# Performance work log

Hardware: AMD Instinct MI355X
Metric: run time of the kernel (lower is better)

Reference implementation:

```python
import jax, jax.numpy as jnp
import numpy as np

N_HEADS = 16


def _rope_table(seq_len, head_dim):
    # Matches RotaryPositionalEmbedding: emb = cat(sin(pos*inv_freq), cos(pos*inv_freq))
    inv_freq = 1.0 / (10000.0 ** (jnp.arange(0, head_dim, 2, dtype=jnp.float32) / head_dim))
    sinusoid = jnp.arange(seq_len, dtype=jnp.float32)[:, None] * inv_freq[None, :]  # [S, hd/2]
    return jnp.sin(sinusoid), jnp.cos(sinusoid)


def _apply_rope(q, k, seq_len, head_dim):
    # Faithful to the torch code, which slices emb[:, :hd/2] (== sin) and calls it 'cos',
    # and emb[:, hd/2:] (== cos) and calls it 'sin'. We keep that exact math.
    sin_tab, cos_tab = _rope_table(seq_len, head_dim)
    c = sin_tab[None, None]  # named 'cos' in torch code, actually sin values
    s = cos_tab[None, None]  # named 'sin' in torch code, actually cos values
    half = head_dim // 2
    def rot(x):
        x1, x2 = x[..., :half], x[..., half:]
        return jnp.concatenate([x1 * c - x2 * s, x2 * c + x1 * s], axis=-1)
    return rot(q), rot(k)


def setup_inputs() -> dict:
    key = jax.random.key(0)
    ks = jax.random.split(key, 9)
    B, S, D = 4, 2048, 1024
    sc = 1.0 / np.sqrt(D)
    return {
        'hidden_states': jax.random.normal(ks[0], (B, S, D), jnp.float32),
        'Wq': jax.random.normal(ks[1], (D, D), jnp.float32) * sc,
        'bq': jax.random.normal(ks[2], (D,), jnp.float32) * 0.01,
        'Wk': jax.random.normal(ks[3], (D, D), jnp.float32) * sc,
        'bk': jax.random.normal(ks[4], (D,), jnp.float32) * 0.01,
        'Wv': jax.random.normal(ks[5], (D, D), jnp.float32) * sc,
        'bv': jax.random.normal(ks[6], (D,), jnp.float32) * 0.01,
        'Wo': jax.random.normal(ks[7], (D, D), jnp.float32) * sc,
        'bo': jax.random.normal(ks[8], (D,), jnp.float32) * 0.01,
    }


def reference(hidden_states, Wq, bq, Wk, bk, Wv, bv, Wo, bo):
    B, S, D = hidden_states.shape
    H = N_HEADS
    hd = D // H

    def proj(W, b):
        y = jnp.einsum('bsd,ed->bse', hidden_states, W) + b  # nn.Linear: x @ W.T + b
        return y.reshape(B, S, H, hd).transpose(0, 2, 1, 3)   # [B,H,S,hd]

    q = proj(Wq, bq)
    k = proj(Wk, bk)
    v = proj(Wv, bv)
    q, k = _apply_rope(q, k, S, hd)

    scale = 1.0 / np.sqrt(hd)
    scores = jnp.einsum('bhqd,bhkd->bhqk', q, k) * scale  # [B,H,S,S]
    attn = jax.nn.softmax(scores, axis=-1)
    ctx = jnp.einsum('bhqk,bhkd->bhqd', attn, v)          # [B,H,S,hd]
    ctx = ctx.transpose(0, 2, 1, 3).reshape(B, S, D)
    return jnp.einsum('bsd,ed->bse', ctx, Wo) + bo
```

## Files before the change

### kernel.cpp

```cpp
#include <hip/hip_runtime.h>
#include <math.h>

#define SEQ 2048
#define DMODEL 1024
#define NH 16
#define HD 64
#define BH 64
#define MROWS 8192
#define QKV_U16 8388608
#define LOG2E 1.4426950408889634f

typedef __attribute__((ext_vector_type(8))) _Float16 half8;
typedef __attribute__((ext_vector_type(4))) _Float16 half4;
typedef __attribute__((ext_vector_type(2))) __fp16 fp16v2;
typedef __attribute__((ext_vector_type(8))) short short8;
typedef __attribute__((ext_vector_type(4))) float floatx4;
typedef unsigned short ush;

union FH { _Float16 h; ush u; };
union PK { fp16v2 v; unsigned u; };
union PH { unsigned u[2]; half4 h; };

__device__ inline ush f2h(float x) { FH c; c.h = (_Float16)x; return c.u; }

__device__ inline void glds16(const ush* g, ush* l) {
  __builtin_amdgcn_global_load_lds((const __attribute__((address_space(1))) void*)g,
                                   (__attribute__((address_space(3))) void*)l, 16, 0, 0);
}

__global__ __launch_bounds__(256)
void cvt_kb(const float* __restrict__ src, ush* __restrict__ dst, int M) {
  __shared__ float T[64][33];
  const int t = threadIdx.x;
  const int k0 = blockIdx.x * 32, m0 = blockIdx.y * 64;
  {
    int row = t >> 2, c = (t & 3) * 8;
    const float* sp = src + (size_t)(m0 + row) * DMODEL + k0 + c;
    float4 x0 = *(const float4*)sp;
    float4 x1 = *(const float4*)(sp + 4);
    float xs[8] = {x0.x, x0.y, x0.z, x0.w, x1.x, x1.y, x1.z, x1.w};
#pragma unroll
    for (int j = 0; j < 8; ++j) T[row][c + j] = xs[j];
  }
  __syncthreads();
  const int ml = t & 63, kbl = t >> 6;
  short8 h8;
#pragma unroll
  for (int j = 0; j < 8; ++j) h8[j] = (short)f2h(T[ml][kbl * 8 + j]);
  *(short8*)(dst + ((size_t)(k0 / 8 + kbl) * M + m0 + ml) * 8) = h8;
}

__global__ __launch_bounds__(256)
void cvt_w4(const float* __restrict__ W0, const float* __restrict__ W1,
            const float* __restrict__ W2, const float* __restrict__ W3,
            ush* __restrict__ dst) {
  __shared__ float T[64][33];
  const int z = blockIdx.z;
  const float* src = (z == 0) ? W0 : (z == 1) ? W1 : (z == 2) ? W2 : W3;
  ush* dz = dst + (size_t)z * DMODEL * DMODEL;
  const int t = threadIdx.x;
  const int k0 = blockIdx.x * 32, m0 = blockIdx.y * 64;
  {
    int row = t >> 2, c = (t & 3) * 8;
    const float* sp = src + (size_t)(m0 + row) * DMODEL + k0 + c;
    float4 x0 = *(const float4*)sp;
    float4 x1 = *(const float4*)(sp + 4);
    float xs[8] = {x0.x, x0.y, x0.z, x0.w, x1.x, x1.y, x1.z, x1.w};
#pragma unroll
    for (int j = 0; j < 8; ++j) T[row][c + j] = xs[j];
  }
  __syncthreads();
  const int ml = t & 63, kbl = t >> 6;
  short8 h8;
#pragma unroll
  for (int j = 0; j < 8; ++j) h8[j] = (short)f2h(T[ml][kbl * 8 + j]);
  *(short8*)(dz + ((size_t)(k0 / 8 + kbl) * DMODEL + m0 + ml) * 8) = h8;
}

__global__ __launch_bounds__(256)
void sincos_kernel(float2* __restrict__ tab) {
  const int idx = blockIdx.x * 256 + threadIdx.x;
  const int s = idx >> 5, i = idx & 31;
  const float f = (float)pow(10000.0, -(double)i / 32.0);
  const float ang = (float)s * f;
  tab[idx] = make_float2(sinf(ang), cosf(ang));
}

template<int QKV>
__global__ __launch_bounds__(256, 4)
void gemm_f16(const ush* __restrict__ A, const ush* __restrict__ W0,
              const float* __restrict__ b0, const float* __restrict__ b1,
              const float* __restrict__ b2, void* __restrict__ out0,
              void* __restrict__ out1, void* __restrict__ out2,
              const float2* __restrict__ sctab) {
  constexpr int BN = QKV ? 128 : 64;
  constexpr int TN = QKV ? 4 : 2;
  __shared__ ush SA[2][4096];
  __shared__ ush SW[2][BN * 32];
  const int tid  = threadIdx.x;
  const int wave = tid >> 6;
  const int lane = tid & 63;
  const int fr = lane & 15;
  const int fg = lane >> 4;
  const int wm = wave & 1;
  const int wn = wave >> 1;

  const int zz = QKV ? (blockIdx.x >> 3) : 3;
  const int nx = QKV ? (blockIdx.x & 7) : blockIdx.x;
  const int m0 = blockIdx.y * 128;
  const int n0 = nx * BN;
  const int m_base = m0 + wm * 64;
  const int n_base = n0 + wn * (TN * 16);

  const ush* W = W0 + (size_t)(QKV ? zz : 0) * (DMODEL * DMODEL);
  const float* bias = QKV ? (zz == 0 ? b0 : zz == 1 ? b1 : b2) : b0;
  void* outp = QKV ? (zz == 0 ? out0 : zz == 1 ? out1 : out2) : out0;
  const float scale = (QKV && zz == 0) ? 0.125f * LOG2E : 1.0f;

  floatx4 acc[4][TN];
#pragma unroll
  for (int i = 0; i < 4; ++i)
#pragma unroll
    for (int j = 0; j < TN; ++j) acc[i][j] = (floatx4){0.f, 0.f, 0.f, 0.f};

  auto stage = [&](int b, int kb0) {
#pragma unroll
    for (int p = 0; p < 2; ++p) {
      const int eb = p * 256 + wave * 64;
      const int kb = eb >> 7, r0 = eb & 127;
      const ush* ga = A + (size_t)(kb0 + kb) * (MROWS * 8) + (size_t)(m0 + r0 + lane) * 8;
      glds16(ga, &SA[b][(size_t)eb * 8]);
    }
    if (QKV) {
#pragma unroll
      for (int p = 0; p < 2; ++p) {
        const int eb = p * 256 + wave * 64;
        const int kb = eb >> 7, r0 = eb & 127;
        const ush* gw = W + (size_t)(kb0 + kb) * (DMODEL * 8) + (size_t)(n0 + r0 + lane) * 8;
        glds16(gw, &SW[b][(size_t)eb * 8]);
      }
    } else {
      const ush* gw = W + (size_t)(kb0 + wave) * (DMODEL * 8) + (size_t)(n0 + lane) * 8;
      glds16(gw, &SW[b][(size_t)wave * 512]);
    }
  };

  auto compute = [&](int b) {
    const int kbl = fg;
    half8 ah[4], wh[TN];
#pragma unroll
    for (int tm = 0; tm < 4; ++tm)
      ah[tm] = *(const half8*)&SA[b][(size_t)(kbl * 128 + wm * 64 + tm * 16 + fr) * 8];
#pragma unroll
    for (int tn = 0; tn < TN; ++tn)
      wh[tn] = *(const half8*)&SW[b][(size_t)(kbl * BN + wn * (TN * 16) + tn * 16 + fr) * 8];
#pragma unroll
    for (int tm = 0; tm < 4; ++tm)
#pragma unroll
      for (int tn = 0; tn < TN; ++tn)
        acc[tm][tn] = __builtin_amdgcn_mfma_f32_16x16x32_f16(ah[tm], wh[tn], acc[tm][tn], 0, 0, 0);
  };

  stage(0, 0);
  __syncthreads();
  for (int t = 0; t < 32; ++t) {
    if (t + 1 < 32) stage((t + 1) & 1, (t + 1) * 4);
    compute(t & 1);
    __syncthreads();
  }

  float bias_s[TN];
#pragma unroll
  for (int tn = 0; tn < TN; ++tn) bias_s[tn] = bias[n_base + tn * 16 + fr];

  if (!QKV) {
#pragma unroll
    for (int tm = 0; tm < 4; ++tm)
#pragma unroll
      for (int tn = 0; tn < TN; ++tn)
#pragma unroll
        for (int r = 0; r < 4; ++r) {
          const int m = m_base + tm * 16 + fg * 4 + r;
          const int n = n_base + tn * 16 + fr;
          ((float*)outp)[(size_t)m * DMODEL + n] = acc[tm][tn][r] + bias_s[tn];
        }
    return;
  }

  const int h = (n_base >> 6) & 15;
  ush* out = (ush*)outp;

  if (zz == 2) {
#pragma unroll
    for (int tm = 0; tm < 4; ++tm)
#pragma unroll
      for (int tn = 0; tn < 4; ++tn)
#pragma unroll
        for (int r = 0; r < 4; ++r) {
          const int m = m_base + tm * 16 + fg * 4 + r;
          const int s = m & (SEQ - 1);
          const size_t bh = (size_t)((m >> 11) * NH + h);
          const int d = tn * 16 + fr;
          const int k6 = s & 63, ktl = s >> 6;
          const int s2 = k6 >> 5;
          const int jj = ((k6 >> 4) & 1) * 4 + (k6 & 3);
          const int fgv = (k6 >> 2) & 3;
          const int dt = d >> 4, frv = d & 15;
          size_t pos = ((((bh * 32 + ktl) * 4 + dt) * 2 + s2) * 64 + fgv * 16 + frv) * 8 + jj;
          out[pos] = f2h(acc[tm][tn][r] + bias_s[tn]);
        }
    return;
  }

#pragma unroll
  for (int tn2 = 0; tn2 < 2; ++tn2) {
    const int i = tn2 * 16 + fr;
#pragma unroll
    for (int tm = 0; tm < 4; ++tm)
#pragma unroll
      for (int r = 0; r < 4; ++r) {
        const int m = m_base + tm * 16 + fg * 4 + r;
        const int s = m & (SEQ - 1);
        const size_t bh = (size_t)((m >> 11) * NH + h);
        const float x1 = acc[tm][tn2][r] + bias_s[tn2];
        const float x2 = acc[tm][tn2 + 2][r] + bias_s[tn2 + 2];
        const float2 sc = sctab[(s << 5) + i];
        const float sv = sc.x, cv = sc.y;
        const float o1 = (x1 * sv - x2 * cv) * scale;
        const float o2 = (x2 * sv + x1 * cv) * scale;
        const int d1 = i, d2 = i + 32;
#pragma unroll
        for (int e = 0; e < 2; ++e) {
          const int d = e ? d2 : d1;
          const float ov = e ? o2 : o1;
          const int ks = d >> 5, fgq = (d >> 3) & 3, j = d & 7;
          size_t pos;
          if (zz == 0) {
            const int qt = s >> 5, mm = (s >> 4) & 1, fr2 = s & 15;
            pos = ((((bh * 64 + qt) * 2 + mm) * 2 + ks) * 64 + fgq * 16 + fr2) * 8 + j;
          } else {
            const int ktl = s >> 6, jt = (s >> 4) & 3, fr2 = s & 15;
            pos = ((((bh * 32 + ktl) * 4 + jt) * 2 + ks) * 64 + fgq * 16 + fr2) * 8 + j;
          }
          out[pos] = f2h(ov);
        }
      }
  }
}

__global__ __launch_bounds__(256, 2)
void flash_mfma(const ush* __restrict__ qsw, const ush* __restrict__ ksw,
                const ush* __restrict__ vsw, ush* __restrict__ ctxf) {
  __shared__ __align__(16) ush Tep[4][64][72];
  __shared__ float Lden[4][64];
  const int tid = threadIdx.x;
  const int wave = tid >> 6;
  const int lane = tid & 63;
  const int fr = lane & 15;
  const int fg = lane >> 4;

  const int lin = blockIdx.x + 8 * blockIdx.y;
  const int xcd = lin & 7;
  const int t2  = lin >> 3;
  const int qblk = t2 & 7;
  const int bh   = xcd + 8 * (t2 >> 3);

  const int q0 = qblk * 256 + wave * 64;
  const ush* qp = qsw + ((size_t)bh * 64 + (q0 >> 5)) * 2048;
  const ush* kp = ksw + (size_t)bh * 131072;
  const ush* vp = vsw + (size_t)bh * 131072;

  half8 qf[4][2];
#pragma unroll
  for (int qn = 0; qn < 4; ++qn)
#pragma unroll
    for (int ks = 0; ks < 2; ++ks)
      qf[qn][ks] = *(const half8*)(qp + (qn * 2 + ks) * 512 + lane * 8);

  floatx4 oacc[4][4];
#pragma unroll
  for (int qn = 0; qn < 4; ++qn)
#pragma unroll
    for (int i = 0; i < 4; ++i) oacc[qn][i] = (floatx4){0.f, 0.f, 0.f, 0.f};
  float lsum[4] = {0.f, 0.f, 0.f, 0.f};

  const fp16v2 one2 = {(__fp16)1.0f, (__fp16)1.0f};

  for (int kt = 0; kt < 32; ++kt) {
    const ush* ktp = kp + kt * 4096;
    const ush* vtp = vp + kt * 4096;

    half8 kf[8], vf[8];
#pragma unroll
    for (int i = 0; i < 8; ++i) kf[i] = *(const half8*)(ktp + i * 512 + lane * 8);
#pragma unroll
    for (int i = 0; i < 8; ++i) vf[i] = *(const half8*)(vtp + i * 512 + lane * 8);

#pragma unroll
    for (int qn = 0; qn < 4; ++qn) {
      floatx4 s4[4];
#pragma unroll
      for (int jt = 0; jt < 4; ++jt) s4[jt] = (floatx4){0.f, 0.f, 0.f, 0.f};
      __builtin_amdgcn_s_setprio(1);
#pragma unroll
      for (int ks = 0; ks < 2; ++ks)
#pragma unroll
        for (int jt = 0; jt < 4; ++jt)
          s4[jt] = __builtin_amdgcn_mfma_f32_16x16x32_f16(kf[jt * 2 + ks], qf[qn][ks], s4[jt], 0, 0, 0);
      __builtin_amdgcn_s_setprio(0);

      half4 P[4];
#pragma unroll
      for (int jt = 0; jt < 4; ++jt) {
        float p0 = __builtin_amdgcn_exp2f(s4[jt][0]);
        float p1 = __builtin_amdgcn_exp2f(s4[jt][1]);
        float p2 = __builtin_amdgcn_exp2f(s4[jt][2]);
        float p3 = __builtin_amdgcn_exp2f(s4[jt][3]);
        PK a, b;
        a.v = __builtin_amdgcn_cvt_pkrtz(p0, p1);
        b.v = __builtin_amdgcn_cvt_pkrtz(p2, p3);
        lsum[qn] = __builtin_amdgcn_fdot2(a.v, one2, lsum[qn], false);
        lsum[qn] = __builtin_amdgcn_fdot2(b.v, one2, lsum[qn], false);
        PH ph; ph.u[0] = a.u; ph.u[1] = b.u;
        P[jt] = ph.h;
      }

      __builtin_amdgcn_s_setprio(1);
#pragma unroll
      for (int s2 = 0; s2 < 2; ++s2) {
        half8 p8 = __builtin_shufflevector(P[s2 * 2], P[s2 * 2 + 1], 0, 1, 2, 3, 4, 5, 6, 7);
#pragma unroll
        for (int dt = 0; dt < 4; ++dt)
          oacc[qn][dt] = __builtin_amdgcn_mfma_f32_16x16x32_f16(p8, vf[dt * 2 + s2], oacc[qn][dt], 0, 0, 0);
      }
      __builtin_amdgcn_s_setprio(0);
    }
  }

#pragma unroll
  for (int qn = 0; qn < 4; ++qn) {
    lsum[qn] += __shfl_xor(lsum[qn], 16);
    lsum[qn] += __shfl_xor(lsum[qn], 32);
    Lden[wave][qn * 16 + fr] = lsum[qn];
  }

  const int b = bh >> 4, h = bh & 15;
#pragma unroll
  for (int qn = 0; qn < 4; ++qn)
#pragma unroll
    for (int r = 0; r < 4; ++r) {
      const float inv = 1.0f / Lden[wave][qn * 16 + fg * 4 + r];
#pragma unroll
      for (int dt = 0; dt < 4; ++dt)
        Tep[wave][qn * 16 + fg * 4 + r][dt * 16 + fr] = f2h(oacc[qn][dt][r] * inv);
    }
  const size_t mrow0 = (size_t)b * SEQ + q0;
  const int kb = lane >> 3;
#pragma unroll
  for (int i = 0; i < 8; ++i) {
    const int q = (lane & 7) + i * 8;
    short8 v = *(const short8*)&Tep[wave][q][kb * 8];
    *(short8*)(ctxf + ((size_t)(h * 8 + kb) * MROWS + mrow0 + q) * 8) = v;
  }
}

extern "C" void kernel_launch(void* const* d_in, const int* in_sizes, int n_in,
                              void* d_out, int out_size, void* d_ws, size_t ws_size,
                              hipStream_t stream) {
  const float* hs = (const float*)d_in[0];
  const float* Wq = (const float*)d_in[1];
  const float* bq = (const float*)d_in[2];
  const float* Wk = (const float*)d_in[3];
  const float* bk = (const float*)d_in[4];
  const float* Wv = (const float*)d_in[5];
  const float* bv = (const float*)d_in[6];
  const float* Wo = (const float*)d_in[7];
  const float* bo = (const float*)d_in[8];

  ush* qsw  = (ush*)d_ws;
  ush* ksw  = qsw + QKV_U16;
  ush* vsw  = ksw + QKV_U16;
  ush* hsf  = vsw + QKV_U16;
  ush* ctxf = hsf + QKV_U16;
  ush* Wf4  = ctxf + QKV_U16;
  float2* sctab = (float2*)(Wf4 + 4 * DMODEL * DMODEL);

  const size_t WS = (size_t)DMODEL * DMODEL;

  sincos_kernel<<<256, 256, 0, stream>>>(sctab);
  cvt_w4<<<dim3(32, 16, 4), 256, 0, stream>>>(Wq, Wk, Wv, Wo, Wf4);
  cvt_kb<<<dim3(32, 128), 256, 0, stream>>>(hs, hsf, MROWS);

  gemm_f16<1><<<dim3(24, 64), 256, 0, stream>>>(hsf, Wf4, bq, bk, bv,
                                                qsw, ksw, vsw, sctab);

  flash_mfma<<<dim3(8, BH), 256, 0, stream>>>(qsw, ksw, vsw, ctxf);

  gemm_f16<0><<<dim3(16, 64), 256, 0, stream>>>(ctxf, Wf4 + 3 * WS, bo, nullptr, nullptr,
                                                d_out, nullptr, nullptr, sctab);
}
```

Measured before the change: 286.1 us.

## Triple-buffer GEMM K-loop, retile output GEMM, halve flash query tile per wave

The GEMM main loop moves from a double-buffered loop with full __syncthreads to a three-stage LDS ring. It uses explicit vmcnt waits and raw s_barrier so two tiles of global-to-LDS loads stay in flight during compute. The output projection GEMM is retiled to 64x128 blocks on a 8x128 grid, and the QKV GEMM occupancy hint drops to 3 to fit the extra LDS buffer. The flash attention kernel gives each wave 32 queries instead of 64 and doubles the grid, with a launch-bounds occupancy of 4, to raise parallelism and occupancy. The cost is more K/V reloads per query and more blocks.

```diff
diff --git a/kernel.cpp b/kernel.cpp
--- a/kernel.cpp
+++ b/kernel.cpp
@@ -87,28 +87,29 @@
 }
 
 template<int QKV>
-__global__ __launch_bounds__(256, 4)
+__global__ __launch_bounds__(256, QKV ? 3 : 4)
 void gemm_f16(const ush* __restrict__ A, const ush* __restrict__ W0,
               const float* __restrict__ b0, const float* __restrict__ b1,
               const float* __restrict__ b2, void* __restrict__ out0,
               void* __restrict__ out1, void* __restrict__ out2,
               const float2* __restrict__ sctab) {
-  constexpr int BN = QKV ? 128 : 64;
+  constexpr int BM = QKV ? 128 : 64;
   constexpr int TN = QKV ? 4 : 2;
-  __shared__ ush SA[2][4096];
-  __shared__ ush SW[2][BN * 32];
+  constexpr int NT = 32;
+  __shared__ ush SA[3][BM * 32];
+  __shared__ ush SW[3][4096];
   const int tid  = threadIdx.x;
   const int wave = tid >> 6;
   const int lane = tid & 63;
   const int fr = lane & 15;
   const int fg = lane >> 4;
-  const int wm = wave & 1;
-  const int wn = wave >> 1;
+  const int wm = QKV ? (wave & 1) : 0;
+  const int wn = QKV ? (wave >> 1) : wave;
 
   const int zz = QKV ? (blockIdx.x >> 3) : 3;
   const int nx = QKV ? (blockIdx.x & 7) : blockIdx.x;
-  const int m0 = blockIdx.y * 128;
-  const int n0 = nx * BN;
+  const int m0 = blockIdx.y * BM;
+  const int n0 = nx * 128;
   const int m_base = m0 + wm * 64;
   const int n_base = n0 + wn * (TN * 16);
 
@@ -123,25 +124,22 @@
 #pragma unroll
     for (int j = 0; j < TN; ++j) acc[i][j] = (floatx4){0.f, 0.f, 0.f, 0.f};
 
-  auto stage = [&](int b, int kb0) {
+  auto stage = [&](int b, int kt) {
+    const int kb0 = kt * 4;
+#pragma unroll
+    for (int p = 0; p < (QKV ? 2 : 1); ++p) {
+      const int c = p * 256 + wave * 64;
+      const int kb = QKV ? (c >> 7) : (c >> 6);
+      const int r0 = c & (BM - 1);
+      glds16(A + (size_t)(kb0 + kb) * (MROWS * 8) + (size_t)(m0 + r0 + lane) * 8,
+             &SA[b][(size_t)c * 8]);
+    }
 #pragma unroll
     for (int p = 0; p < 2; ++p) {
-      const int eb = p * 256 + wave * 64;
-      const int kb = eb >> 7, r0 = eb & 127;
-      const ush* ga = A + (size_t)(kb0 + kb) * (MROWS * 8) + (size_t)(m0 + r0 + lane) * 8;
-      glds16(ga, &SA[b][(size_t)eb * 8]);
-    }
-    if (QKV) {
-#pragma unroll
-      for (int p = 0; p < 2; ++p) {
-        const int eb = p * 256 + wave * 64;
-        const int kb = eb >> 7, r0 = eb & 127;
-        const ush* gw = W + (size_t)(kb0 + kb) * (DMODEL * 8) + (size_t)(n0 + r0 + lane) * 8;
-        glds16(gw, &SW[b][(size_t)eb * 8]);
-      }
-    } else {
-      const ush* gw = W + (size_t)(kb0 + wave) * (DMODEL * 8) + (size_t)(n0 + lane) * 8;
-      glds16(gw, &SW[b][(size_t)wave * 512]);
+      const int c = p * 256 + wave * 64;
+      const int kb = c >> 7, r0 = c & 127;
+      glds16(W + (size_t)(kb0 + kb) * (DMODEL * 8) + (size_t)(n0 + r0 + lane) * 8,
+             &SW[b][(size_t)c * 8]);
     }
   };
 
@@ -150,10 +148,10 @@
     half8 ah[4], wh[TN];
 #pragma unroll
     for (int tm = 0; tm < 4; ++tm)
-      ah[tm] = *(const half8*)&SA[b][(size_t)(kbl * 128 + wm * 64 + tm * 16 + fr) * 8];
+      ah[tm] = *(const half8*)&SA[b][(size_t)(kbl * BM + wm * 64 + tm * 16 + fr) * 8];
 #pragma unroll
     for (int tn = 0; tn < TN; ++tn)
-      wh[tn] = *(const half8*)&SW[b][(size_t)(kbl * BN + wn * (TN * 16) + tn * 16 + fr) * 8];
+      wh[tn] = *(const half8*)&SW[b][(size_t)(kbl * 128 + wn * (TN * 16) + tn * 16 + fr) * 8];
 #pragma unroll
     for (int tm = 0; tm < 4; ++tm)
 #pragma unroll
@@ -162,11 +160,30 @@
   };
 
   stage(0, 0);
-  __syncthreads();
-  for (int t = 0; t < 32; ++t) {
-    if (t + 1 < 32) stage((t + 1) & 1, (t + 1) * 4);
-    compute(t & 1);
-    __syncthreads();
+  stage(1, 1);
+  if constexpr (QKV) asm volatile("s_waitcnt vmcnt(4)" ::: "memory");
+  else               asm volatile("s_waitcnt vmcnt(3)" ::: "memory");
+  __builtin_amdgcn_s_barrier();
+  __builtin_amdgcn_sched_barrier(0);
+
+  int bc = 0;
+  for (int t = 0; t < NT; ++t) {
+    if (t + 2 < NT) {
+      int bs = bc + 2; if (bs >= 3) bs -= 3;
+      stage(bs, t + 2);
+    }
+    compute(bc);
+    if (t + 1 < NT) {
+      if (t + 2 < NT) {
+        if constexpr (QKV) asm volatile("s_waitcnt vmcnt(4)" ::: "memory");
+        else               asm volatile("s_waitcnt vmcnt(3)" ::: "memory");
+      } else {
+        asm volatile("s_waitcnt vmcnt(0)" ::: "memory");
+      }
+      __builtin_amdgcn_s_barrier();
+      __builtin_amdgcn_sched_barrier(0);
+    }
+    ++bc; if (bc == 3) bc = 0;
   }
 
   float bias_s[TN];
@@ -194,7 +211,7 @@
 #pragma unroll
     for (int tm = 0; tm < 4; ++tm)
 #pragma unroll
-      for (int tn = 0; tn < 4; ++tn)
+      for (int tn = 0; tn < TN; ++tn)
 #pragma unroll
         for (int r = 0; r < 4; ++r) {
           const int m = m_base + tm * 16 + fg * 4 + r;
@@ -248,41 +265,41 @@
   }
 }
 
-__global__ __launch_bounds__(256, 2)
+__global__ __launch_bounds__(256, 4)
 void flash_mfma(const ush* __restrict__ qsw, const ush* __restrict__ ksw,
                 const ush* __restrict__ vsw, ush* __restrict__ ctxf) {
-  __shared__ __align__(16) ush Tep[4][64][72];
-  __shared__ float Lden[4][64];
+  __shared__ __align__(16) ush Tep[4][32][72];
+  __shared__ float Lden[4][32];
   const int tid = threadIdx.x;
   const int wave = tid >> 6;
   const int lane = tid & 63;
   const int fr = lane & 15;
   const int fg = lane >> 4;
 
-  const int lin = blockIdx.x + 8 * blockIdx.y;
+  const int lin = blockIdx.x + 16 * blockIdx.y;
   const int xcd = lin & 7;
   const int t2  = lin >> 3;
-  const int qblk = t2 & 7;
-  const int bh   = xcd + 8 * (t2 >> 3);
-
-  const int q0 = qblk * 256 + wave * 64;
+  const int qblk = t2 & 15;
+  const int bh   = xcd + 8 * (t2 >> 4);
+
+  const int q0 = qblk * 128 + wave * 32;
   const ush* qp = qsw + ((size_t)bh * 64 + (q0 >> 5)) * 2048;
   const ush* kp = ksw + (size_t)bh * 131072;
   const ush* vp = vsw + (size_t)bh * 131072;
 
-  half8 qf[4][2];
-#pragma unroll
-  for (int qn = 0; qn < 4; ++qn)
+  half8 qf[2][2];
+#pragma unroll
+  for (int qn = 0; qn < 2; ++qn)
 #pragma unroll
     for (int ks = 0; ks < 2; ++ks)
       qf[qn][ks] = *(const half8*)(qp + (qn * 2 + ks) * 512 + lane * 8);
 
-  floatx4 oacc[4][4];
-#pragma unroll
-  for (int qn = 0; qn < 4; ++qn)
+  floatx4 oacc[2][4];
+#pragma unroll
+  for (int qn = 0; qn < 2; ++qn)
 #pragma unroll
     for (int i = 0; i < 4; ++i) oacc[qn][i] = (floatx4){0.f, 0.f, 0.f, 0.f};
-  float lsum[4] = {0.f, 0.f, 0.f, 0.f};
+  float lsum[2] = {0.f, 0.f};
 
   const fp16v2 one2 = {(__fp16)1.0f, (__fp16)1.0f};
 
@@ -297,7 +314,7 @@
     for (int i = 0; i < 8; ++i) vf[i] = *(const half8*)(vtp + i * 512 + lane * 8);
 
 #pragma unroll
-    for (int qn = 0; qn < 4; ++qn) {
+    for (int qn = 0; qn < 2; ++qn) {
       floatx4 s4[4];
 #pragma unroll
       for (int jt = 0; jt < 4; ++jt) s4[jt] = (floatx4){0.f, 0.f, 0.f, 0.f};
@@ -338,7 +355,7 @@
   }
 
 #pragma unroll
-  for (int qn = 0; qn < 4; ++qn) {
+  for (int qn = 0; qn < 2; ++qn) {
     lsum[qn] += __shfl_xor(lsum[qn], 16);
     lsum[qn] += __shfl_xor(lsum[qn], 32);
     Lden[wave][qn * 16 + fr] = lsum[qn];
@@ -346,7 +363,7 @@
 
   const int b = bh >> 4, h = bh & 15;
 #pragma unroll
-  for (int qn = 0; qn < 4; ++qn)
+  for (int qn = 0; qn < 2; ++qn)
 #pragma unroll
     for (int r = 0; r < 4; ++r) {
       const float inv = 1.0f / Lden[wave][qn * 16 + fg * 4 + r];
@@ -357,7 +374,7 @@
   const size_t mrow0 = (size_t)b * SEQ + q0;
   const int kb = lane >> 3;
 #pragma unroll
-  for (int i = 0; i < 8; ++i) {
+  for (int i = 0; i < 4; ++i) {
     const int q = (lane & 7) + i * 8;
     short8 v = *(const short8*)&Tep[wave][q][kb * 8];
     *(short8*)(ctxf + ((size_t)(h * 8 + kb) * MROWS + mrow0 + q) * 8) = v;
@@ -394,8 +411,8 @@
   gemm_f16<1><<<dim3(24, 64), 256, 0, stream>>>(hsf, Wf4, bq, bk, bv,
                                                 qsw, ksw, vsw, sctab);
 
-  flash_mfma<<<dim3(8, BH), 256, 0, stream>>>(qsw, ksw, vsw, ctxf);
-
-  gemm_f16<0><<<dim3(16, 64), 256, 0, stream>>>(ctxf, Wf4 + 3 * WS, bo, nullptr, nullptr,
+  flash_mfma<<<dim3(16, BH), 256, 0, stream>>>(qsw, ksw, vsw, ctxf);
+
+  gemm_f16<0><<<dim3(8, 128), 256, 0, stream>>>(ctxf, Wf4 + 3 * WS, bo, nullptr, nullptr,
                                                 d_out, nullptr, nullptr, sctab);
 }
```

After: 301.5 us. 1.05x slower.
